# Optimization experiments

Measured on AMD Instinct MI355X. Metric: run time of the kernel, lower is better.

## Reference

```python
import jax, jax.numpy as jnp
import numpy as np

H = 768; I = 3072; NH = 12; HD = H // NH; L = 2; V = 32000
N = 2048; NSUB = 8; SUBLEN = 256; WIDTH = 512; EPS = 1e-6


def rmsnorm(x, w):
    x32 = x.astype(jnp.float32)
    n = x32 * jax.lax.rsqrt(jnp.mean(x32 * x32, axis=-1, keepdims=True) + EPS)
    return (n * w).astype(x.dtype)


def fixed_pos_embedding(ages, dim):
    # inv_freq: [dim//2]; torch.linspace(0, 2, steps=dim//2)
    inv_freq = 1.0 / (10000.0 ** jnp.linspace(0.0, 2.0, dim // 2))
    t = ages[:, None] * inv_freq[None, :]              # [N, dim//2]
    # stack((s, s), -1).reshape -> duplicate each entry pairwise (interleaved)
    sin = jnp.repeat(jnp.sin(t), 2, axis=-1)[:, None, :]  # [N, 1, dim]
    cos = jnp.repeat(jnp.cos(t), 2, axis=-1)[:, None, :]
    return sin, cos


def apply_rope(x, sin, cos):
    # x: [N, heads, hd]; sin/cos: [N, 1, hd]
    x1 = x[..., 0::2]
    x2 = x[..., 1::2]
    rot = jnp.stack((-x2, x1), axis=-1).reshape(x.shape)
    return x * cos + rot * sin


def build_mask(subject_lengths, n):
    # block-diagonal (per subject) + causal local window of WIDTH
    csum = jnp.cumsum(subject_lengths)
    idx = jnp.arange(n)
    seg = jnp.searchsorted(csum, idx, side='right')   # subject id per token
    i = idx[:, None]; j = idx[None, :]
    same = seg[:, None] == seg[None, :]
    return same & (j <= i) & ((i - j) < WIDTH)        # [N, N] bool


def encoder_layer(x, time_data, sin, cos, mask, norm_w, W_in, W_out):
    h = rmsnorm(x, norm_w)
    all_time = jnp.concatenate((time_data, time_data ** 2), axis=-1)  # [N, 4]
    h = h.at[:, -all_time.shape[1]:].set(all_time.astype(h.dtype))
    t = h @ W_in                                      # [N, 2I + 3H]
    ff = t[:, : 2 * I]
    qkv = t[:, 2 * I:].reshape(-1, 3, NH, HD)
    q = apply_rope(qkv[:, 0], sin, cos)
    k = apply_rope(qkv[:, 1], sin, cos)
    v = qkv[:, 2]
    scores = jnp.einsum('qhd,khd->hqk', q, k) / jnp.sqrt(jnp.float32(HD))
    scores = jnp.where(mask[None, :, :], scores, -jnp.inf)
    probs = jax.nn.softmax(scores, axis=-1)
    attn = jnp.einsum('hqk,khd->qhd', probs, v).reshape(-1, H)
    x1, x2 = jnp.split(ff, 2, axis=-1)
    ffo = jax.nn.silu(x1) * x2                        # swiglu
    return jnp.concatenate((attn, ffo), axis=-1) @ W_out


def setup_inputs() -> dict:
    key = jax.random.key(0)
    ks = jax.random.split(key, 6)
    tokens = jax.random.randint(ks[0], (N,), 0, V)
    ages = jnp.sort(jax.random.uniform(ks[1], (N,), dtype=jnp.float32) * 100.0)
    time_data = jax.random.normal(ks[2], (N, 2), dtype=jnp.float32)
    subject_lengths = jnp.full((NSUB,), SUBLEN, dtype=jnp.int32)
    embed_table = jax.random.normal(ks[3], (V, H), dtype=jnp.float32) * 0.02
    in_norm_w = jnp.ones((H,), jnp.float32)
    out_norm_w = jnp.ones((H,), jnp.float32)
    layer_norm_w = jnp.ones((L, H), jnp.float32)
    layer_Win = jax.random.normal(ks[4], (L, H, 2 * I + 3 * H), dtype=jnp.float32) / np.sqrt(H)
    layer_Wout = jax.random.normal(ks[5], (L, H + I, H), dtype=jnp.float32) / np.sqrt(H + I)
    return dict(tokens=tokens, ages=ages, time_data=time_data,
                subject_lengths=subject_lengths, embed_table=embed_table,
                in_norm_w=in_norm_w, out_norm_w=out_norm_w,
                layer_norm_w=layer_norm_w, layer_Win=layer_Win, layer_Wout=layer_Wout)


def reference(tokens, ages, time_data, subject_lengths, embed_table,
              in_norm_w, out_norm_w, layer_norm_w, layer_Win, layer_Wout):
    x = embed_table[tokens]                           # [N, H]
    x = rmsnorm(x, in_norm_w)
    sin, cos = fixed_pos_embedding(ages, HD)
    mask = build_mask(subject_lengths, x.shape[0])
    for l in range(L):
        x = x + encoder_layer(x, time_data, sin, cos, mask,
                              layer_norm_w[l], layer_Win[l], layer_Wout[l])
    return rmsnorm(x, out_norm_w)
```

## Files before the change

kernel.cpp:

```cpp
#include <hip/hip_runtime.h>
#include <math.h>

typedef unsigned short ushort_t;
typedef float f32x4 __attribute__((ext_vector_type(4)));
typedef __bf16 bf16x8 __attribute__((ext_vector_type(8)));

#define DEVFN __device__ __forceinline__

DEVFN ushort_t f2bf(float f) {
  unsigned int u = __float_as_uint(f);
  u += 0x7FFFu + ((u >> 16) & 1u);
  return (ushort_t)(u >> 16);
}
DEVFN float bf2f(ushort_t u) { return __uint_as_float((unsigned int)u << 16); }

DEVFN void gload(const ushort_t* src, char* dst) {
  __builtin_amdgcn_global_load_lds(
      (const __attribute__((address_space(1))) unsigned int*)src,
      (__attribute__((address_space(3))) unsigned int*)dst, 16, 0, 0);
}

#define N_TOK  2048
#define HDIM   768
#define TCOLS  8448
#define FFI    3072
#define NHEADS 12
#define HD     64
#define NSEG   8
#define SEGLEN 256
#define ABCOLS 3840
#define NPART  6
#define KCHUNK 768

__global__ __launch_bounds__(256) void preamble(
    const float* __restrict__ Win, const float* __restrict__ Wout,
    ushort_t* __restrict__ winT, ushort_t* __restrict__ woutT,
    const float* __restrict__ embed, const int* __restrict__ tokens,
    const float* __restrict__ ages,
    const float* __restrict__ in_nw, const float* __restrict__ layer_nw,
    const float* __restrict__ time_data,
    float* __restrict__ x, ushort_t* __restrict__ hbuf, float2* __restrict__ sctab) {
  const int tid = threadIdx.x;
  if (blockIdx.x < 9216) {
    __shared__ ushort_t tile[32][66];
    int id = blockIdx.x;
    const float* in; ushort_t* out; int R, C, tr, tc;
    if (id < 6336) {
      const int z = id / 3168; id -= z * 3168;
      R = HDIM; C = TCOLS;
      tr = (id / 264) * 64; tc = (id % 264) * 32;
      in = Win + (size_t)z * R * C; out = winT + (size_t)z * R * C;
    } else {
      id -= 6336;
      const int z = id / 1440; id -= z * 1440;
      R = ABCOLS; C = HDIM;
      tr = (id / 24) * 64; tc = (id % 24) * 32;
      in = Wout + (size_t)z * R * C; out = woutT + (size_t)z * R * C;
    }
    const int tx = tid & 31, ty = tid >> 5;
#pragma unroll
    for (int i = 0; i < 8; ++i) {
      const int r = ty + i * 8;
      tile[tx][r] = f2bf(in[(size_t)(tr + r) * C + tc + tx]);
    }
    __syncthreads();
#pragma unroll
    for (int i = 0; i < 4; ++i) {
      const int c = ty + i * 8;
      ushort2 pk; pk.x = tile[c][2 * tx]; pk.y = tile[c][2 * tx + 1];
      *(ushort2*)(out + (size_t)(tc + c) * R + tr + 2 * tx) = pk;
    }
    return;
  }
  const int row = blockIdx.x - 9216;
  if (tid < 32) {
    const int k = tid;
    const float e = (2.0f * (float)k) / 31.0f;
    const float t = ages[row] * expf(-e * logf(10000.0f));
    float2 cs; cs.x = cosf(t); cs.y = sinf(t);
    sctab[row * HD + 2 * k] = cs;
    sctab[row * HD + 2 * k + 1] = cs;
  }
  __shared__ float part[4];
  const float* src = embed + (size_t)tokens[row] * HDIM;
  float4 v = {0.f, 0.f, 0.f, 0.f};
  const int c0 = tid * 4;
  if (tid < 192) v = *(const float4*)(src + c0);
  float ss = v.x * v.x + v.y * v.y + v.z * v.z + v.w * v.w;
#pragma unroll
  for (int off = 1; off < 64; off <<= 1) ss += __shfl_xor(ss, off);
  if ((tid & 63) == 0) part[tid >> 6] = ss;
  __syncthreads();
  const float rs = rsqrtf((part[0] + part[1] + part[2] + part[3]) * (1.0f / HDIM) + 1e-6f);
  float4 y = {0.f, 0.f, 0.f, 0.f};
  if (tid < 192) {
    y.x = v.x * rs * in_nw[c0]; y.y = v.y * rs * in_nw[c0 + 1];
    y.z = v.z * rs * in_nw[c0 + 2]; y.w = v.w * rs * in_nw[c0 + 3];
    *(float4*)(x + (size_t)row * HDIM + c0) = y;
  }
  float ss2 = y.x * y.x + y.y * y.y + y.z * y.z + y.w * y.w;
#pragma unroll
  for (int off = 1; off < 64; off <<= 1) ss2 += __shfl_xor(ss2, off);
  __syncthreads();
  if ((tid & 63) == 0) part[tid >> 6] = ss2;
  __syncthreads();
  const float rs2 = rsqrtf((part[0] + part[1] + part[2] + part[3]) * (1.0f / HDIM) + 1e-6f);
  if (tid < 192) {
    float val[4];
#pragma unroll
    for (int j = 0; j < 4; ++j) {
      const int c = c0 + j;
      float vv = ((const float*)&y)[j] * rs2 * layer_nw[c];
      if (c >= HDIM - 4) {
        const float td = time_data[row * 2 + (c & 1)];
        vv = (c >= HDIM - 2) ? td * td : td;
      }
      val[j] = vv;
    }
    ushort4 pk;
    pk.x = f2bf(val[0]); pk.y = f2bf(val[1]); pk.z = f2bf(val[2]); pk.w = f2bf(val[3]);
    *(ushort4*)(hbuf + (size_t)row * HDIM + c0) = pk;
  }
}

__global__ __launch_bounds__(256) void rms_fused(
    const ushort_t* __restrict__ cpartb, float* __restrict__ x,
    const float* __restrict__ w, const float* __restrict__ time_data,
    float* __restrict__ out_f32, ushort_t* __restrict__ out_bf16, const int mode) {
  const int row = blockIdx.x;
  const size_t stride = (size_t)N_TOK * HDIM;
  const int tid = threadIdx.x;
  const int c0 = tid * 4;
  float4 s = {0.f, 0.f, 0.f, 0.f};
  if (tid < 192) {
    s = *(const float4*)(x + (size_t)row * HDIM + c0);
#pragma unroll
    for (int z = 0; z < NPART; ++z) {
      const ushort4 p = *(const ushort4*)(cpartb + z * stride + (size_t)row * HDIM + c0);
      s.x += bf2f(p.x); s.y += bf2f(p.y); s.z += bf2f(p.z); s.w += bf2f(p.w);
    }
    if (mode == 1) *(float4*)(x + (size_t)row * HDIM + c0) = s;
  }
  float ss = s.x * s.x + s.y * s.y + s.z * s.z + s.w * s.w;
#pragma unroll
  for (int off = 1; off < 64; off <<= 1) ss += __shfl_xor(ss, off);
  __shared__ float part[4];
  if ((tid & 63) == 0) part[tid >> 6] = ss;
  __syncthreads();
  const float rs = rsqrtf((part[0] + part[1] + part[2] + part[3]) * (1.0f / HDIM) + 1e-6f);
  if (tid < 192) {
    float val[4];
#pragma unroll
    for (int j = 0; j < 4; ++j) {
      const int c = c0 + j;
      float vv = ((const float*)&s)[j] * rs * w[c];
      if (mode == 1 && c >= HDIM - 4) {
        const float td = time_data[row * 2 + (c & 1)];
        vv = (c >= HDIM - 2) ? td * td : td;
      }
      val[j] = vv;
    }
    if (mode == 1) {
      ushort4 pk;
      pk.x = f2bf(val[0]); pk.y = f2bf(val[1]); pk.z = f2bf(val[2]); pk.w = f2bf(val[3]);
      *(ushort4*)(out_bf16 + (size_t)row * HDIM + c0) = pk;
    } else {
      float4 o; o.x = val[0]; o.y = val[1]; o.z = val[2]; o.w = val[3];
      *(float4*)(out_f32 + (size_t)row * HDIM + c0) = o;
    }
  }
}

#define G1_NT 24
#define G1_ABYT 8192
#define G1_BUF  20480

DEVFN int swz64(int p) {
  const int g = ((p >> 6) & 3) ^ ((p >> 8) & 3);
  return p ^ (g << 4);
}
DEVFN int ffmap(int vr) {
  return (vr < 2 * FFI) ? ((((vr >> 4) & 1) * FFI) + ((vr >> 5) << 4) + (vr & 15)) : vr;
}

DEVFN void g1f_stage(const ushort_t* __restrict__ A, const ushort_t* __restrict__ BT,
                     int m0, int n0, int kt_el, char* buf, int tid) {
#pragma unroll
  for (int i = 0; i < 2; ++i) {
    const int q = swz64(i * 4096 + tid * 16);
    gload(A + (size_t)(m0 + (q >> 6)) * HDIM + kt_el + ((q & 63) >> 1),
          buf + i * 4096 + ((tid >> 6) << 10));
  }
#pragma unroll
  for (int i = 0; i < 3; ++i) {
    const int q = swz64(i * 4096 + tid * 16);
    const int vr = n0 + (q >> 6);
    gload(BT + (size_t)ffmap(vr) * HDIM + kt_el + ((q & 63) >> 1),
          buf + G1_ABYT + i * 4096 + ((tid >> 6) << 10));
  }
}

__global__ __launch_bounds__(256, 3) void gemm1f(
    const ushort_t* __restrict__ A, const ushort_t* __restrict__ BT,
    const float2* __restrict__ sctab,
    ushort_t* __restrict__ ab, ushort_t* __restrict__ qr,
    ushort_t* __restrict__ kr, ushort_t* __restrict__ vT) {
  __shared__ __align__(16) char smem[2 * G1_BUF];
  const int tid = threadIdx.x;
  const int l = tid & 63, l15 = l & 15, l4 = l >> 4;
  const int wid = tid >> 6, wr = wid >> 1, wc = wid & 1;
  const int bid = (int)blockIdx.x;
  const int wg = (bid & 7) * 88 + (bid >> 3);
  const int nt = wg >> 4, mt = wg & 15;
  const int m0 = mt * 128, n0 = nt * 192;

  f32x4 acc[4][6] = {};

  g1f_stage(A, BT, m0, n0, 0,  smem, tid);
  g1f_stage(A, BT, m0, n0, 32, smem + G1_BUF, tid);
  asm volatile("s_waitcnt vmcnt(5)" ::: "memory");
  __builtin_amdgcn_s_barrier();
  __builtin_amdgcn_sched_barrier(0);

  for (int t = 0; t < G1_NT; ++t) {
    const char* bufA = smem + (t & 1) * G1_BUF;
    const char* bufB = bufA + G1_ABYT;
    bf16x8 a4[4], b6[6];
#pragma unroll
    for (int m = 0; m < 4; ++m) {
      const int p = (wr * 64 + m * 16 + l15) * 64 + l4 * 16;
      a4[m] = *(const bf16x8*)(bufA + swz64(p));
    }
#pragma unroll
    for (int n = 0; n < 6; ++n) {
      const int p = (wc * 96 + n * 16 + l15) * 64 + l4 * 16;
      b6[n] = *(const bf16x8*)(bufB + swz64(p));
    }
#pragma unroll
    for (int m = 0; m < 4; ++m)
#pragma unroll
      for (int n = 0; n < 6; ++n)
        acc[m][n] = __builtin_amdgcn_mfma_f32_16x16x32_bf16(a4[m], b6[n], acc[m][n], 0, 0, 0);

    if (t == G1_NT - 1) break;
    __builtin_amdgcn_sched_barrier(0);
    __builtin_amdgcn_s_barrier();
    if (t + 2 < G1_NT) {
      g1f_stage(A, BT, m0, n0, (t + 2) * 32, smem + (t & 1) * G1_BUF, tid);
      asm volatile("s_waitcnt vmcnt(5)" ::: "memory");
    } else {
      asm volatile("s_waitcnt vmcnt(0)" ::: "memory");
    }
    __builtin_amdgcn_s_barrier();
    __builtin_amdgcn_sched_barrier(0);
  }

  if (nt < 32) {
#pragma unroll
    for (int m = 0; m < 4; ++m)
#pragma unroll
      for (int np = 0; np < 3; ++np) {
        const int colj = (nt * 6 + wc * 3 + np) * 16 + l15;
#pragma unroll
        for (int r = 0; r < 4; ++r) {
          const float x1 = acc[m][2 * np][r], x2 = acc[m][2 * np + 1][r];
          const float sv = x1 / (1.f + __expf(-x1)) * x2;
          const int row = m0 + wr * 64 + m * 16 + l4 * 4 + r;
          ab[(size_t)row * ABCOLS + HDIM + colj] = f2bf(sv);
        }
      }
  } else {
#pragma unroll
    for (int n = 0; n < 6; ++n) {
      const int gcol = (nt - 32) * 192 + wc * 96 + n * 16;
      const int g = gcol >> 6;
      const int typ = g / NHEADS, h = g - typ * NHEADS;
      const int d = (gcol & 63) + l15;
      if (typ == 2) {
#pragma unroll
        for (int m = 0; m < 4; ++m) {
          ushort4 pk;
          pk.x = f2bf(acc[m][n][0]); pk.y = f2bf(acc[m][n][1]);
          pk.z = f2bf(acc[m][n][2]); pk.w = f2bf(acc[m][n][3]);
          const int row0 = m0 + wr * 64 + m * 16 + l4 * 4;
          *(ushort4*)(vT + ((size_t)h * HD + d) * N_TOK + row0) = pk;
        }
      } else {
        ushort_t* dst = (typ == 0) ? qr : kr;
        const float sgn = (l15 & 1) ? 1.f : -1.f;
#pragma unroll
        for (int m = 0; m < 4; ++m)
#pragma unroll
          for (int r = 0; r < 4; ++r) {
            const float val = acc[m][n][r];
            const float partner = __shfl_xor(val, 1);
            const int row = m0 + wr * 64 + m * 16 + l4 * 4 + r;
            const float2 cs = sctab[row * HD + d];
            dst[((size_t)h * N_TOK + row) * HD + d] = f2bf(val * cs.x + sgn * partner * cs.y);
          }
      }
    }
  }
}

#define G2_BUF 40960

DEVFN int swz128(int p) { return p ^ (((p >> 7) & 7) << 4); }

DEVFN void g2_stage(const ushort_t* __restrict__ A, const ushort_t* __restrict__ BT,
                    int m0, int n0, int kt_el, char* buf, int tid) {
#pragma unroll
  for (int i = 0; i < 10; ++i) {
    const int p = i * 4096 + tid * 16;
    const bool isA = p < 16384;
    const int q = swz128(isA ? p : p - 16384);
    const int row = q >> 7, colel = (q & 127) >> 1;
    const ushort_t* src = (isA ? A + (size_t)(m0 + row) * ABCOLS
                               : BT + (size_t)(n0 + row) * ABCOLS) + kt_el + colel;
    gload(src, buf + i * 4096 + ((tid >> 6) << 10));
  }
}

DEVFN void g2_body(const ushort_t* __restrict__ A, const ushort_t* __restrict__ BT,
                   char* smem, int m0, int n0, int kt0, int NT,
                   ushort_t* __restrict__ outp, int tid) {
  const int l = tid & 63, l15 = l & 15, l4 = l >> 4;
  const int w = tid >> 6, wr = w >> 1, wc = w & 1;
  f32x4 acc[4][6] = {};

  g2_stage(A, BT, m0, n0, kt0, smem, tid);
  g2_stage(A, BT, m0, n0, kt0 + 64, smem + G2_BUF, tid);
  asm volatile("s_waitcnt vmcnt(10)" ::: "memory");
  __builtin_amdgcn_s_barrier();
  __builtin_amdgcn_sched_barrier(0);

  for (int t = 0; t < NT; ++t) {
    const char* bufA = smem + (t & 1) * G2_BUF;
    const char* bufB = bufA + 16384;
#pragma unroll
    for (int kk = 0; kk < 2; ++kk) {
      bf16x8 af[4], bv[6];
#pragma unroll
      for (int mi = 0; mi < 4; ++mi) {
        const int p = (wr * 64 + mi * 16 + l15) * 128 + kk * 64 + l4 * 16;
        af[mi] = *(const bf16x8*)(bufA + swz128(p));
      }
#pragma unroll
      for (int ni = 0; ni < 6; ++ni) {
        const int p = (wc * 96 + ni * 16 + l15) * 128 + kk * 64 + l4 * 16;
        bv[ni] = *(const bf16x8*)(bufB + swz128(p));
      }
#pragma unroll
      for (int mi = 0; mi < 4; ++mi)
#pragma unroll
        for (int ni = 0; ni < 6; ++ni)
          acc[mi][ni] = __builtin_amdgcn_mfma_f32_16x16x32_bf16(af[mi], bv[ni], acc[mi][ni], 0, 0, 0);
    }

    if (t == NT - 1) break;
    __builtin_amdgcn_sched_barrier(0);
    __builtin_amdgcn_s_barrier();
    if (t + 2 < NT) {
      g2_stage(A, BT, m0, n0, kt0 + (t + 2) * 64, smem + (t & 1) * G2_BUF, tid);
      asm volatile("s_waitcnt vmcnt(10)" ::: "memory");
    } else {
      asm volatile("s_waitcnt vmcnt(0)" ::: "memory");
    }
    __builtin_amdgcn_s_barrier();
    __builtin_amdgcn_sched_barrier(0);
  }

#pragma unroll
  for (int mi = 0; mi < 4; ++mi)
#pragma unroll
    for (int ni = 0; ni < 6; ++ni)
#pragma unroll
      for (int r = 0; r < 4; ++r) {
        const int row = m0 + wr * 64 + mi * 16 + l4 * 4 + r;
        const int col = n0 + wc * 96 + ni * 16 + l15;
        outp[(size_t)row * HDIM + col] = f2bf(acc[mi][ni][r]);
      }
}

DEVFN void attn_one(const ushort_t* __restrict__ qr, const ushort_t* __restrict__ kr,
                    const ushort_t* __restrict__ vT, ushort_t* __restrict__ ab,
                    int h, int seg, int qt, ushort_t* Pw, int l15, int l4) {
  const int qrow0 = seg * SEGLEN + qt * 16;
  bf16x8 aq[2];
#pragma unroll
  for (int kk = 0; kk < 2; ++kk)
    aq[kk] = *(const bf16x8*)(qr + ((size_t)h * N_TOK + qrow0 + l15) * HD + kk * 32 + l4 * 8);

  f32x4 o[4] = {};
  float m_run[4], l_run[4];
#pragma unroll
  for (int r = 0; r < 4; ++r) { m_run[r] = -1e30f; l_run[r] = 0.f; }

  const int kbmax = qt >> 2;
  for (int kb = 0; kb <= kbmax; ++kb) {
    bf16x8 bk[4][2];
#pragma unroll
    for (int ni = 0; ni < 4; ++ni)
#pragma unroll
      for (int kk = 0; kk < 2; ++kk)
        bk[ni][kk] = *(const bf16x8*)(kr + ((size_t)h * N_TOK + seg * SEGLEN + kb * 64 + ni * 16 + l15) * HD + kk * 32 + l4 * 8);
    f32x4 s[4] = {};
#pragma unroll
    for (int ni = 0; ni < 4; ++ni)
#pragma unroll
      for (int kk = 0; kk < 2; ++kk)
        s[ni] = __builtin_amdgcn_mfma_f32_16x16x32_bf16(aq[kk], bk[ni][kk], s[ni], 0, 0, 0);

    const bool diag = (kb == kbmax);
#pragma unroll
    for (int ni = 0; ni < 4; ++ni)
#pragma unroll
      for (int r = 0; r < 4; ++r) {
        float v = s[ni][r] * 0.125f;
        if (diag) {
          const int qrow = qt * 16 + l4 * 4 + r;
          const int jcol = kb * 64 + ni * 16 + l15;
          if (jcol > qrow) v = -1e30f;
        }
        s[ni][r] = v;
      }

    float sc_[4];
#pragma unroll
    for (int r = 0; r < 4; ++r) {
      float pm = fmaxf(fmaxf(s[0][r], s[1][r]), fmaxf(s[2][r], s[3][r]));
      pm = fmaxf(pm, __shfl_xor(pm, 1));
      pm = fmaxf(pm, __shfl_xor(pm, 2));
      pm = fmaxf(pm, __shfl_xor(pm, 4));
      pm = fmaxf(pm, __shfl_xor(pm, 8));
      const float mn = fmaxf(m_run[r], pm);
      sc_[r] = __expf(m_run[r] - mn);
      m_run[r] = mn;
    }
#pragma unroll
    for (int ni = 0; ni < 4; ++ni)
#pragma unroll
      for (int r = 0; r < 4; ++r)
        s[ni][r] = __expf(s[ni][r] - m_run[r]);
#pragma unroll
    for (int r = 0; r < 4; ++r) {
      float ls = s[0][r] + s[1][r] + s[2][r] + s[3][r];
      ls += __shfl_xor(ls, 1);
      ls += __shfl_xor(ls, 2);
      ls += __shfl_xor(ls, 4);
      ls += __shfl_xor(ls, 8);
      l_run[r] = l_run[r] * sc_[r] + ls;
    }
#pragma unroll
    for (int ni = 0; ni < 4; ++ni)
#pragma unroll
      for (int r = 0; r < 4; ++r)
        o[ni][r] *= sc_[r];

#pragma unroll
    for (int ni = 0; ni < 4; ++ni)
#pragma unroll
      for (int r = 0; r < 4; ++r)
        Pw[(l4 * 4 + r) * 64 + ni * 16 + l15] = f2bf(s[ni][r]);

    bf16x8 pa[2], bv[4][2];
#pragma unroll
    for (int k2 = 0; k2 < 2; ++k2)
      pa[k2] = *(const bf16x8*)(&Pw[l15 * 64 + k2 * 32 + l4 * 8]);
#pragma unroll
    for (int ni = 0; ni < 4; ++ni)
#pragma unroll
      for (int k2 = 0; k2 < 2; ++k2)
        bv[ni][k2] = *(const bf16x8*)(vT + ((size_t)h * HD + ni * 16 + l15) * N_TOK + seg * SEGLEN + kb * 64 + k2 * 32 + l4 * 8);
#pragma unroll
    for (int ni = 0; ni < 4; ++ni)
#pragma unroll
      for (int k2 = 0; k2 < 2; ++k2)
        o[ni] = __builtin_amdgcn_mfma_f32_16x16x32_bf16(pa[k2], bv[ni][k2], o[ni], 0, 0, 0);
  }

#pragma unroll
  for (int ni = 0; ni < 4; ++ni)
#pragma unroll
    for (int r = 0; r < 4; ++r) {
      const int row = qrow0 + l4 * 4 + r;
      const int col = h * HD + ni * 16 + l15;
      ab[(size_t)row * ABCOLS + col] = f2bf(o[ni][r] / l_run[r]);
    }
}

__global__ __launch_bounds__(256, 2) void fused_mid(
    const ushort_t* __restrict__ ab, const ushort_t* __restrict__ woutT,
    ushort_t* __restrict__ cpartb,
    const ushort_t* __restrict__ qr, const ushort_t* __restrict__ kr,
    const ushort_t* __restrict__ vT, ushort_t* __restrict__ ab_out) {
  __shared__ __align__(16) char smem[2 * G2_BUF];
  const int b = (int)blockIdx.x;
  const int tid = threadIdx.x;
  const int sel = b % 7;
  if (sel < 3) {
    const int a = (b / 7) * 3 + sel;
    const int h = a % NHEADS;
    const int r2 = a / NHEADS;
    const int seg = r2 & 7, p = r2 >> 3;
    const int w = tid >> 6, l = tid & 63;
    const int l15 = l & 15, l4 = l >> 4;
    ushort_t* Pw = (ushort_t*)smem + w * (16 * 64);
    attn_one(qr, kr, vT, ab_out, h, seg, p * 4 + w, Pw, l15, l4);
    attn_one(qr, kr, vT, ab_out, h, seg, (3 - p) * 4 + w, Pw, l15, l4);
  } else {
    const int f = (b / 7) * 4 + (sel - 3);
    const int z = 1 + (f >> 6);
    const int rem = f & 63;
    const int n0 = (rem & 3) * 192, m0 = (rem >> 2) * 128;
    g2_body(ab, woutT, smem, m0, n0, z * KCHUNK, 12,
            cpartb + (size_t)(z - 1) * N_TOK * HDIM, tid);
  }
}

__global__ __launch_bounds__(256, 2) void gemm2_z0(
    const ushort_t* __restrict__ ab, const ushort_t* __restrict__ woutT,
    ushort_t* __restrict__ cpartb) {
  __shared__ __align__(16) char smem[2 * G2_BUF];
  const int b = (int)blockIdx.x;
  const int half = b >> 6, rem = b & 63;
  const int n0 = (rem & 3) * 192, m0 = (rem >> 2) * 128;
  g2_body(ab, woutT, smem, m0, n0, half * 384, 6,
          cpartb + (size_t)(4 + half) * N_TOK * HDIM, threadIdx.x);
}

extern "C" void kernel_launch(void* const* d_in, const int* in_sizes, int n_in,
                              void* d_out, int out_size, void* d_ws, size_t ws_size,
                              hipStream_t stream) {
  const int*   tokens   = (const int*)d_in[0];
  const float* ages     = (const float*)d_in[1];
  const float* time_d   = (const float*)d_in[2];
  const float* embed    = (const float*)d_in[4];
  const float* in_nw    = (const float*)d_in[5];
  const float* out_nw   = (const float*)d_in[6];
  const float* layer_nw = (const float*)d_in[7];
  const float* Win      = (const float*)d_in[8];
  const float* Wout     = (const float*)d_in[9];
  float* out = (float*)d_out;

  char* ws = (char*)d_ws;
  float*    x      = (float*)   (ws + 0);
  ushort_t* hbuf   = (ushort_t*)(ws + 6291456);
  float2*   sctab  = (float2*)  (ws + 9437184);
  ushort_t* cpartb = (ushort_t*)(ws + 10485760);
  ushort_t* ab     = (ushort_t*)(ws + 29360128);
  ushort_t* qrb    = (ushort_t*)(ws + 45088768);
  ushort_t* krb    = (ushort_t*)(ws + 48234496);
  ushort_t* vTb    = (ushort_t*)(ws + 51380224);
  ushort_t* winT   = (ushort_t*)(ws + 54525952);
  ushort_t* woutT  = (ushort_t*)(ws + 80478208);

  preamble<<<dim3(11264), dim3(256), 0, stream>>>(Win, Wout, winT, woutT,
                                                  embed, tokens, ages, in_nw, layer_nw,
                                                  time_d, x, hbuf, sctab);

  for (int lyr = 0; lyr < 2; ++lyr) {
    gemm1f<<<dim3(704), dim3(256), 0, stream>>>(hbuf, winT + (size_t)lyr * TCOLS * HDIM,
                                                sctab, ab, qrb, krb, vTb);
    fused_mid<<<dim3(448), dim3(256), 0, stream>>>(ab, woutT + (size_t)lyr * HDIM * ABCOLS,
                                                   cpartb, qrb, krb, vTb, ab);
    gemm2_z0<<<dim3(128), dim3(256), 0, stream>>>(ab, woutT + (size_t)lyr * HDIM * ABCOLS,
                                                  cpartb);
    if (lyr == 0)
      rms_fused<<<dim3(N_TOK), dim3(256), 0, stream>>>(cpartb, x, layer_nw + HDIM, time_d,
                                                       nullptr, hbuf, 1);
    else
      rms_fused<<<dim3(N_TOK), dim3(256), 0, stream>>>(cpartb, x, out_nw, nullptr,
                                                       out, nullptr, 2);
  }
}
```

Before: 184.1 us.

## Overlap weight transpose/convert work with layer-0 GEMM and attention kernels

The preamble now transposes and converts only the layer-0 Win. The layer-0 Wout, layer-1 Win and layer-1 Wout transposes run as extra blocks appended to the layer-0 gemm1f and fused_mid launches. The goal is to hide the bandwidth-bound conversion work behind compute-bound kernels and shorten the serial preamble. The risk is that the extra blocks compete for CUs and bandwidth, or get scheduled after the main blocks and lengthen those kernels. Correctness relies on each converted weight being written by a launch that finishes before the launch that reads it.

```diff
diff --git a/kernel.cpp b/kernel.cpp
--- a/kernel.cpp
+++ b/kernel.cpp
@@ -32,47 +32,39 @@
 #define NPART  6
 #define KCHUNK 768
 
+DEVFN void transpose_tile(const float* __restrict__ in, ushort_t* __restrict__ out,
+                          int R, int C, int tr, int tc, int tid, char* smem) {
+  ushort_t (*tile)[66] = (ushort_t(*)[66])smem;
+  const int tx = tid & 31, ty = tid >> 5;
+#pragma unroll
+  for (int i = 0; i < 8; ++i) {
+    const int r = ty + i * 8;
+    tile[tx][r] = f2bf(in[(size_t)(tr + r) * C + tc + tx]);
+  }
+  __syncthreads();
+#pragma unroll
+  for (int i = 0; i < 4; ++i) {
+    const int c = ty + i * 8;
+    ushort2 pk; pk.x = tile[c][2 * tx]; pk.y = tile[c][2 * tx + 1];
+    *(ushort2*)(out + (size_t)(tc + c) * R + tr + 2 * tx) = pk;
+  }
+}
+
 __global__ __launch_bounds__(256) void preamble(
-    const float* __restrict__ Win, const float* __restrict__ Wout,
-    ushort_t* __restrict__ winT, ushort_t* __restrict__ woutT,
+    const float* __restrict__ Win, ushort_t* __restrict__ winT,
     const float* __restrict__ embed, const int* __restrict__ tokens,
     const float* __restrict__ ages,
     const float* __restrict__ in_nw, const float* __restrict__ layer_nw,
     const float* __restrict__ time_data,
     float* __restrict__ x, ushort_t* __restrict__ hbuf, float2* __restrict__ sctab) {
   const int tid = threadIdx.x;
-  if (blockIdx.x < 9216) {
-    __shared__ ushort_t tile[32][66];
-    int id = blockIdx.x;
-    const float* in; ushort_t* out; int R, C, tr, tc;
-    if (id < 6336) {
-      const int z = id / 3168; id -= z * 3168;
-      R = HDIM; C = TCOLS;
-      tr = (id / 264) * 64; tc = (id % 264) * 32;
-      in = Win + (size_t)z * R * C; out = winT + (size_t)z * R * C;
-    } else {
-      id -= 6336;
-      const int z = id / 1440; id -= z * 1440;
-      R = ABCOLS; C = HDIM;
-      tr = (id / 24) * 64; tc = (id % 24) * 32;
-      in = Wout + (size_t)z * R * C; out = woutT + (size_t)z * R * C;
-    }
-    const int tx = tid & 31, ty = tid >> 5;
-#pragma unroll
-    for (int i = 0; i < 8; ++i) {
-      const int r = ty + i * 8;
-      tile[tx][r] = f2bf(in[(size_t)(tr + r) * C + tc + tx]);
-    }
-    __syncthreads();
-#pragma unroll
-    for (int i = 0; i < 4; ++i) {
-      const int c = ty + i * 8;
-      ushort2 pk; pk.x = tile[c][2 * tx]; pk.y = tile[c][2 * tx + 1];
-      *(ushort2*)(out + (size_t)(tc + c) * R + tr + 2 * tx) = pk;
-    }
+  if (blockIdx.x < 3168) {
+    __shared__ char tsmem[32 * 66 * 2];
+    const int id = blockIdx.x;
+    transpose_tile(Win, winT, HDIM, TCOLS, (id / 264) * 64, (id % 264) * 32, tid, tsmem);
     return;
   }
-  const int row = blockIdx.x - 9216;
+  const int row = blockIdx.x - 3168;
   if (tid < 32) {
     const int k = tid;
     const float e = (2.0f * (float)k) / 31.0f;
@@ -204,12 +196,24 @@
     const ushort_t* __restrict__ A, const ushort_t* __restrict__ BT,
     const float2* __restrict__ sctab,
     ushort_t* __restrict__ ab, ushort_t* __restrict__ qr,
-    ushort_t* __restrict__ kr, ushort_t* __restrict__ vT) {
+    ushort_t* __restrict__ kr, ushort_t* __restrict__ vT,
+    const float* __restrict__ tj1_src, ushort_t* __restrict__ tj1_dst,
+    const float* __restrict__ tj2_src, ushort_t* __restrict__ tj2_dst) {
   __shared__ __align__(16) char smem[2 * G1_BUF];
   const int tid = threadIdx.x;
+  const int bid = (int)blockIdx.x;
+  if (bid >= 704) {
+    int e = bid - 704;
+    if (e < 1440)
+      transpose_tile(tj1_src, tj1_dst, ABCOLS, HDIM, (e / 24) * 64, (e % 24) * 32, tid, smem);
+    else {
+      e -= 1440;
+      transpose_tile(tj2_src, tj2_dst, HDIM, TCOLS, (e / 264) * 64, (e % 264) * 32, tid, smem);
+    }
+    return;
+  }
   const int l = tid & 63, l15 = l & 15, l4 = l >> 4;
   const int wid = tid >> 6, wr = wid >> 1, wc = wid & 1;
-  const int bid = (int)blockIdx.x;
   const int wg = (bid & 7) * 88 + (bid >> 3);
   const int nt = wg >> 4, mt = wg & 15;
   const int m0 = mt * 128, n0 = nt * 192;
@@ -493,10 +497,16 @@
     const ushort_t* __restrict__ ab, const ushort_t* __restrict__ woutT,
     ushort_t* __restrict__ cpartb,
     const ushort_t* __restrict__ qr, const ushort_t* __restrict__ kr,
-    const ushort_t* __restrict__ vT, ushort_t* __restrict__ ab_out) {
+    const ushort_t* __restrict__ vT, ushort_t* __restrict__ ab_out,
+    const float* __restrict__ tj_src, ushort_t* __restrict__ tj_dst) {
   __shared__ __align__(16) char smem[2 * G2_BUF];
   const int b = (int)blockIdx.x;
   const int tid = threadIdx.x;
+  if (b >= 448) {
+    const int e = b - 448;
+    transpose_tile(tj_src, tj_dst, ABCOLS, HDIM, (e / 24) * 64, (e % 24) * 32, tid, smem);
+    return;
+  }
   const int sel = b % 7;
   if (sel < 3) {
     const int a = (b / 7) * 3 + sel;
@@ -555,17 +565,29 @@
   ushort_t* winT   = (ushort_t*)(ws + 54525952);
   ushort_t* woutT  = (ushort_t*)(ws + 80478208);
 
-  preamble<<<dim3(11264), dim3(256), 0, stream>>>(Win, Wout, winT, woutT,
-                                                  embed, tokens, ages, in_nw, layer_nw,
-                                                  time_d, x, hbuf, sctab);
+  const size_t winStride  = (size_t)TCOLS * HDIM;
+  const size_t woutStride = (size_t)HDIM * ABCOLS;
+
+  preamble<<<dim3(5216), dim3(256), 0, stream>>>(Win, winT, embed, tokens, ages,
+                                                 in_nw, layer_nw, time_d, x, hbuf, sctab);
 
   for (int lyr = 0; lyr < 2; ++lyr) {
-    gemm1f<<<dim3(704), dim3(256), 0, stream>>>(hbuf, winT + (size_t)lyr * TCOLS * HDIM,
-                                                sctab, ab, qrb, krb, vTb);
-    fused_mid<<<dim3(448), dim3(256), 0, stream>>>(ab, woutT + (size_t)lyr * HDIM * ABCOLS,
-                                                   cpartb, qrb, krb, vTb, ab);
-    gemm2_z0<<<dim3(128), dim3(256), 0, stream>>>(ab, woutT + (size_t)lyr * HDIM * ABCOLS,
-                                                  cpartb);
+    if (lyr == 0) {
+      gemm1f<<<dim3(704 + 4608), dim3(256), 0, stream>>>(
+          hbuf, winT, sctab, ab, qrb, krb, vTb,
+          Wout, woutT, Win + winStride, winT + winStride);
+      fused_mid<<<dim3(448 + 1440), dim3(256), 0, stream>>>(
+          ab, woutT, cpartb, qrb, krb, vTb, ab,
+          Wout + woutStride, woutT + woutStride);
+    } else {
+      gemm1f<<<dim3(704), dim3(256), 0, stream>>>(
+          hbuf, winT + winStride, sctab, ab, qrb, krb, vTb,
+          nullptr, nullptr, nullptr, nullptr);
+      fused_mid<<<dim3(448), dim3(256), 0, stream>>>(
+          ab, woutT + woutStride, cpartb, qrb, krb, vTb, ab,
+          nullptr, nullptr);
+    }
+    gemm2_z0<<<dim3(128), dim3(256), 0, stream>>>(ab, woutT + lyr * woutStride, cpartb);
     if (lyr == 0)
       rms_fused<<<dim3(N_TOK), dim3(256), 0, stream>>>(cpartb, x, layer_nw + HDIM, time_d,
                                                        nullptr, hbuf, 1);
```

Result: faster. 179.4 us (-2.5%).
